# Kernel optimization log

Measured on AMD Instinct MI355X. Metric: run time of the kernel, lower is better.

## Reference

```python
import jax, jax.numpy as jnp
import numpy as np

BN_EPS = 1e-5
DIST_MIN = 1e-8
K = 3


def setup_inputs() -> dict:
    key = jax.random.key(0)
    ks = jax.random.split(key, 6)
    B, Nl, Nh, Ch, Cl, out_ch = 4, 8192, 2048, 256, 128, 256
    in_ch = Ch + Cl
    xyz_low = jax.random.normal(ks[0], (B, Nl, 3), jnp.float32)
    xyz_high = jax.random.normal(ks[1], (B, Nh, 3), jnp.float32)
    feat_low = jax.random.normal(ks[2], (B, Cl, Nl), jnp.float32)
    feat_high = jax.random.normal(ks[3], (B, Ch, Nh), jnp.float32)
    # 1x1 Conv1d params (kernel size 1 -> plain channel-mixing matrix)
    W = jax.random.normal(ks[4], (out_ch, in_ch), jnp.float32) * (1.0 / np.sqrt(in_ch))
    b = jax.random.normal(ks[5], (out_ch,), jnp.float32) * 0.01
    gamma = jnp.ones((out_ch,), jnp.float32)
    beta = jnp.zeros((out_ch,), jnp.float32)
    return {"xyz_low": xyz_low, "xyz_high": xyz_high, "feat_low": feat_low,
            "feat_high": feat_high, "W": W, "b": b, "gamma": gamma, "beta": beta}


def reference(xyz_low, xyz_high, feat_low, feat_high, W, b, gamma, beta):
    # --- pairwise euclidean distances (B, Nl, Nh), like torch.cdist ---
    d2 = (jnp.sum(xyz_low ** 2, -1)[:, :, None]
          + jnp.sum(xyz_high ** 2, -1)[:, None, :]
          - 2.0 * jnp.einsum('bld,bhd->blh', xyz_low, xyz_high))
    d = jnp.sqrt(jnp.maximum(d2, 0.0))
    # --- 3-NN (smallest distances) ---
    _, idx = jax.lax.top_k(-d, K)                      # (B, Nl, K)
    dist = jnp.maximum(jnp.take_along_axis(d, idx, axis=-1), DIST_MIN)
    w = 1.0 / dist
    w = w / jnp.sum(w, axis=-1, keepdims=True)         # (B, Nl, K)
    # --- gather neighbor features and inverse-distance interpolate ---
    f_high_T = jnp.transpose(feat_high, (0, 2, 1))      # (B, Nh, Ch)
    neigh = jax.vmap(lambda f, i: f[i])(f_high_T, idx)  # (B, Nl, K, Ch)
    f_interp = jnp.einsum('blk,blkc->bcl', w, neigh)    # (B, Ch, Nl)
    f_cat = jnp.concatenate([f_interp, feat_low], axis=1)  # (B, Ch+Cl, Nl)
    # --- 1x1 Conv1d + BatchNorm1d (training-mode batch stats) + ReLU ---
    y = jnp.einsum('oc,bcn->bon', W, f_cat) + b[None, :, None]
    mean = jnp.mean(y, axis=(0, 2), keepdims=True)
    var = jnp.var(y, axis=(0, 2), keepdims=True)        # biased, as in torch BN
    yn = (y - mean) * jax.lax.rsqrt(var + BN_EPS)
    return jax.nn.relu(gamma[None, :, None] * yn + beta[None, :, None])
```

## Files before the change

kernel.cpp:

```cpp
#include <hip/hip_runtime.h>

constexpr int B_   = 4;
constexpr int NL   = 8192;
constexpr int NH   = 2048;
constexpr int CH   = 256;
constexpr int CL   = 128;
constexpr int CIN  = 384;
constexpr int COUT = 256;

typedef _Float16 f16;
typedef _Float16 f16x8 __attribute__((ext_vector_type(8)));
typedef float    f32x4 __attribute__((ext_vector_type(4)));

#define INS3F(d, h, B0, B1, B2, I0, I1, I2) do {                             \
    bool c0_ = (d) < (B0), c1_ = (d) < (B1), c2_ = (d) < (B2);               \
    int ni1_ = c0_ ? (I0) : (c1_ ? (h) : (I1));                              \
    int ni2_ = c1_ ? (I1) : (c2_ ? (h) : (I2));                              \
    I0 = c0_ ? (h) : (I0); I1 = ni1_; I2 = ni2_;                             \
    float nb1_ = __builtin_amdgcn_fmed3f(B0, B1, (d));                       \
    float nb2_ = __builtin_amdgcn_fmed3f(B1, B2, (d));                       \
    B0 = fminf(B0, (d)); B1 = nb1_; B2 = nb2_;                               \
} while (0)

__global__ __launch_bounds__(256) void prep_kernel(
    const float* __restrict__ feat_high, const float* __restrict__ Wm,
    f16* __restrict__ fhT, f16* __restrict__ Wh)
{
    __shared__ float tt[32][33];
    const int bid = blockIdx.x, tid = threadIdx.x;

    if (bid < 512) {
        const int tx = tid & 31, ty = tid >> 5;
        #pragma unroll
        for (int k = 0; k < 4; ++k) {
            const int u  = bid * 4 + k;
            const int ub = u >> 9, ut = u & 511;
            const int h0 = (ut & 63) * 32, c0 = (ut >> 6) * 32;
            #pragma unroll
            for (int pp = 0; pp < 4; ++pp)
                tt[ty + pp * 8][tx] =
                    feat_high[((size_t)ub * CH + c0 + ty + pp * 8) * NH + h0 + tx];
            __syncthreads();
            #pragma unroll
            for (int pp = 0; pp < 4; ++pp)
                fhT[((size_t)ub * NH + h0 + ty + pp * 8) * CH + c0 + tx] =
                    (f16)tt[tx][ty + pp * 8];
            __syncthreads();
        }
    } else {
        const int i = (bid - 512) * 256 + tid;
        Wh[i] = (f16)Wm[i];
    }
}

__global__ __launch_bounds__(512) void gemm_kernel(
    const float* __restrict__ xyz_low, const float* __restrict__ xyz_high,
    const float* __restrict__ feat_low, const f16* __restrict__ fhT,
    const f16* __restrict__ Wh, const float* __restrict__ bias,
    f16* __restrict__ yh, float* __restrict__ ps, float* __restrict__ psq)
{
    __shared__ __align__(16) char smraw[51712];
    f16*            As   = (f16*)smraw;
    float4*         pts  = (float4*)smraw;
    float*          md   = (float*)(smraw + 32768);
    unsigned short* mi   = (unsigned short*)(smraw + 39168);
    int*            idxL = (int*)(smraw + 50176);
    float*          wL   = (float*)(smraw + 50944);

    const int bid = blockIdx.x, tid = threadIdx.x;
    const int b = bid >> 7, l0 = (bid & 127) * 64;
    const int lane = tid & 63, w = tid >> 6;

    {
        const float* xh = xyz_high + (size_t)b * NH * 3;
        #pragma unroll
        for (int k = 0; k < 4; ++k) {
            const int h = k * 512 + tid;
            float x = xh[h * 3], yy = xh[h * 3 + 1], z = xh[h * 3 + 2];
            pts[h] = make_float4(x, yy, z, x * x + yy * yy + z * z);
        }
    }
    __syncthreads();
    {
        const float* xl = xyz_low + ((size_t)b * NL + l0 + lane) * 3;
        const float lx = xl[0], ly = xl[1], lz = xl[2];
        const float sl = lx * lx + ly * ly + lz * lz;

        float a0 = 1e30f, a1 = 1e30f, a2 = 1e30f;
        float c0 = 1e30f, c1 = 1e30f, c2 = 1e30f;
        int ia0 = 0, ia1 = 0, ia2 = 0, ic0 = 0, ic1 = 0, ic2 = 0;
        const int hA = w * 256, hB = hA + 128;
        #pragma unroll 4
        for (int i = 0; i < 128; ++i) {
            float4 pA = pts[hA + i];
            float4 pB = pts[hB + i];
            float dA = fmaf(-2.0f, fmaf(lx, pA.x, fmaf(ly, pA.y, lz * pA.z)),
                            sl + pA.w);
            float dB = fmaf(-2.0f, fmaf(lx, pB.x, fmaf(ly, pB.y, lz * pB.z)),
                            sl + pB.w);
            INS3F(dA, hA + i, a0, a1, a2, ia0, ia1, ia2);
            INS3F(dB, hB + i, c0, c1, c2, ic0, ic1, ic2);
        }
        INS3F(c0, ic0, a0, a1, a2, ia0, ia1, ia2);
        INS3F(c1, ic1, a0, a1, a2, ia0, ia1, ia2);
        INS3F(c2, ic2, a0, a1, a2, ia0, ia1, ia2);
        const int cb = lane * 25 + w * 3;
        md[cb] = a0;     mi[cb] = (unsigned short)ia0;
        md[cb + 1] = a1; mi[cb + 1] = (unsigned short)ia1;
        md[cb + 2] = a2; mi[cb + 2] = (unsigned short)ia2;
    }
    __syncthreads();

    if (tid < 64) {
        float e0 = 1e30f, e1 = 1e30f, e2 = 1e30f;
        int j0 = 0, j1 = 0, j2 = 0;
        #pragma unroll
        for (int q = 0; q < 24; ++q) {
            float d = md[tid * 25 + q];
            int  ii = mi[tid * 25 + q];
            INS3F(d, ii, e0, e1, e2, j0, j1, j2);
        }
        float d0 = sqrtf(fmaxf(e0, 0.0f));
        float d1 = sqrtf(fmaxf(e1, 0.0f));
        float d2f = sqrtf(fmaxf(e2, 0.0f));
        float iw0 = 1.0f / fmaxf(d0, 1e-8f);
        float iw1 = 1.0f / fmaxf(d1, 1e-8f);
        float iw2 = 1.0f / fmaxf(d2f, 1e-8f);
        float sum = iw0 + iw1 + iw2;
        idxL[tid] = j0; idxL[64 + tid] = j1; idxL[128 + tid] = j2;
        wL[tid] = iw0 / sum; wL[64 + tid] = iw1 / sum; wL[128 + tid] = iw2 / sum;
    }
    __syncthreads();

    {
        const int p = tid >> 3, q = tid & 7;
        const int j0 = idxL[p], j1 = idxL[64 + p], j2 = idxL[128 + p];
        const float u0 = wL[p], u1 = wL[64 + p], u2 = wL[128 + p];
        const f16* r0 = fhT + ((size_t)b * NH + j0) * CH + q * 32;
        const f16* r1 = fhT + ((size_t)b * NH + j1) * CH + q * 32;
        const f16* r2 = fhT + ((size_t)b * NH + j2) * CH + q * 32;
        #pragma unroll
        for (int j = 0; j < 4; ++j) {
            f16x8 v0 = *(const f16x8*)(r0 + j * 8);
            f16x8 v1 = *(const f16x8*)(r1 + j * 8);
            f16x8 v2 = *(const f16x8*)(r2 + j * 8);
            f16x8 o;
            #pragma unroll
            for (int e = 0; e < 8; ++e)
                o[e] = (f16)(u0 * (float)v0[e] + u1 * (float)v1[e]
                             + u2 * (float)v2[e]);
            *(f16x8*)&As[p * 392 + q * 32 + j * 8] = o;
        }
        const int l = tid & 63, cq = tid >> 6;
        const float* flb = feat_low + ((size_t)b * CL + cq * 16) * NL + l0 + l;
        f16 tmp[16];
        #pragma unroll
        for (int i = 0; i < 16; ++i)
            tmp[i] = (f16)flb[(size_t)i * NL];
        *(f16x8*)&As[l * 392 + 256 + cq * 16]     = *(const f16x8*)&tmp[0];
        *(f16x8*)&As[l * 392 + 256 + cq * 16 + 8] = *(const f16x8*)&tmp[8];
    }
    __syncthreads();

    f32x4 acc[2][4] = {};
    const int kb = (lane >> 4) * 8;
    const int r  = lane & 15;
    #pragma unroll
    for (int kt = 0; kt < 12; ++kt) {
        const int k0 = kt * 32;
        f16x8 a[2], bb[4];
        #pragma unroll
        for (int mi2 = 0; mi2 < 2; ++mi2)
            a[mi2] = *(const f16x8*)&Wh[(size_t)(w * 32 + mi2 * 16 + r) * CIN
                                        + k0 + kb];
        #pragma unroll
        for (int ni = 0; ni < 4; ++ni)
            bb[ni] = *(const f16x8*)&As[(ni * 16 + r) * 392 + k0 + kb];
        #pragma unroll
        for (int mi2 = 0; mi2 < 2; ++mi2)
            #pragma unroll
            for (int ni = 0; ni < 4; ++ni)
                acc[mi2][ni] = __builtin_amdgcn_mfma_f32_16x16x32_f16(
                    a[mi2], bb[ni], acc[mi2][ni], 0, 0, 0);
    }

    const int r4 = (lane >> 4) * 4, cl = lane & 15;
    #pragma unroll
    for (int mi2 = 0; mi2 < 2; ++mi2) {
        #pragma unroll
        for (int j = 0; j < 4; ++j) {
            const int o = w * 32 + mi2 * 16 + r4 + j;
            const float bi = bias[o];
            float s = 0.0f, sq = 0.0f;
            #pragma unroll
            for (int ni = 0; ni < 4; ++ni) {
                acc[mi2][ni][j] += bi;
                float v = acc[mi2][ni][j];
                s += v; sq += v * v;
            }
            #pragma unroll
            for (int m = 1; m < 16; m <<= 1) {
                s  += __shfl_xor(s, m);
                sq += __shfl_xor(sq, m);
            }
            if (cl == 0) {
                ps [o * 512 + bid] = s;
                psq[o * 512 + bid] = sq;
            }
        }
    }
    __syncthreads();

    f16* Ys = (f16*)smraw;
    #pragma unroll
    for (int mi2 = 0; mi2 < 2; ++mi2)
        #pragma unroll
        for (int j = 0; j < 4; ++j) {
            const int o = w * 32 + mi2 * 16 + r4 + j;
            #pragma unroll
            for (int ni = 0; ni < 4; ++ni)
                Ys[o * 72 + cl + ni * 16] = (f16)acc[mi2][ni][j];
        }
    __syncthreads();
    {
        const int o = tid >> 1, half = tid & 1;
        f16* dst = yh + ((size_t)b * COUT + o) * NL + l0 + half * 32;
        #pragma unroll
        for (int j = 0; j < 4; ++j)
            *(f16x8*)(dst + j * 8) = *(const f16x8*)&Ys[o * 72 + half * 32 + j * 8];
    }
}

__global__ __launch_bounds__(256) void stats_apply_kernel(
    const float* __restrict__ ps, const float* __restrict__ psq,
    const f16* __restrict__ yh,
    const float* __restrict__ gamma, const float* __restrict__ beta,
    float* __restrict__ y)
{
    const int o = blockIdx.x, b = blockIdx.y, tid = threadIdx.x;
    const int w = tid >> 6, lane = tid & 63;

    float s = ps[o * 512 + tid] + ps[o * 512 + 256 + tid];
    float q = psq[o * 512 + tid] + psq[o * 512 + 256 + tid];
    #pragma unroll
    for (int m = 32; m > 0; m >>= 1) {
        s += __shfl_down(s, m);
        q += __shfl_down(q, m);
    }
    __shared__ float red[8];
    if (lane == 0) { red[w] = s; red[4 + w] = q; }
    __syncthreads();
    s = red[0] + red[1] + red[2] + red[3];
    q = red[4] + red[5] + red[6] + red[7];
    const float n  = (float)(B_ * NL);
    const float mu = s / n;
    const float rs = rsqrtf(q / n - mu * mu + 1e-5f);
    const float g  = gamma[o], be = beta[o];

    const f16* src = yh + ((size_t)b * COUT + o) * NL;
    float*     dst = y  + ((size_t)b * COUT + o) * NL;
    #pragma unroll
    for (int it = 0; it < 4; ++it) {
        const int base = it * 2048 + tid * 8;
        f16x8 v = *(const f16x8*)(src + base);
        float4 o1, o2;
        o1.x = fmaxf(fmaf(g, ((float)v[0] - mu) * rs, be), 0.0f);
        o1.y = fmaxf(fmaf(g, ((float)v[1] - mu) * rs, be), 0.0f);
        o1.z = fmaxf(fmaf(g, ((float)v[2] - mu) * rs, be), 0.0f);
        o1.w = fmaxf(fmaf(g, ((float)v[3] - mu) * rs, be), 0.0f);
        o2.x = fmaxf(fmaf(g, ((float)v[4] - mu) * rs, be), 0.0f);
        o2.y = fmaxf(fmaf(g, ((float)v[5] - mu) * rs, be), 0.0f);
        o2.z = fmaxf(fmaf(g, ((float)v[6] - mu) * rs, be), 0.0f);
        o2.w = fmaxf(fmaf(g, ((float)v[7] - mu) * rs, be), 0.0f);
        *(float4*)(dst + base)     = o1;
        *(float4*)(dst + base + 4) = o2;
    }
}

extern "C" void kernel_launch(void* const* d_in, const int* in_sizes, int n_in,
                              void* d_out, int out_size, void* d_ws, size_t ws_size,
                              hipStream_t stream)
{
    const float* xyz_low   = (const float*)d_in[0];
    const float* xyz_high  = (const float*)d_in[1];
    const float* feat_low  = (const float*)d_in[2];
    const float* feat_high = (const float*)d_in[3];
    const float* Wm        = (const float*)d_in[4];
    const float* bias      = (const float*)d_in[5];
    const float* gamma     = (const float*)d_in[6];
    const float* beta      = (const float*)d_in[7];
    float* y = (float*)d_out;

    float* ps   = (float*)d_ws;
    float* psq  = ps + (size_t)COUT * 512;
    f16*   Wh   = (f16*)(psq + (size_t)COUT * 512);
    f16*   fhT  = Wh + (size_t)COUT * CIN;
    f16*   yh   = fhT + (size_t)B_ * NH * CH;

    prep_kernel<<<896, 256, 0, stream>>>(feat_high, Wm, fhT, Wh);
    gemm_kernel<<<512, 512, 0, stream>>>(
        xyz_low, xyz_high, feat_low, fhT, Wh, bias, yh, ps, psq);
    stats_apply_kernel<<<dim3(COUT, B_), 256, 0, stream>>>(
        ps, psq, yh, gamma, beta, y);
}
```

Before: 75.82 us.

## Double gemm_kernel block size to 1024 threads and split work across 16 waves

Launches the fused kNN+GEMM kernel with 1024 threads (16 waves) instead of 512, so each wave scans 128 high-res points with a single top-3 chain and handles 16 output channels instead of 32. The merge step now reduces 48 partial candidates per point, and the gather, feat_low load and output store are re-partitioned across the larger block. The aim is more parallelism and latency hiding per block. The cost is a longer serial merge by 64 threads, slightly more LDS, and tighter register limits from the 1024-thread launch bound.

```diff
diff --git a/kernel.cpp b/kernel.cpp
--- a/kernel.cpp
+++ b/kernel.cpp
@@ -53,19 +53,19 @@
     }
 }
 
-__global__ __launch_bounds__(512) void gemm_kernel(
+__global__ __launch_bounds__(1024, 8) void gemm_kernel(
     const float* __restrict__ xyz_low, const float* __restrict__ xyz_high,
     const float* __restrict__ feat_low, const f16* __restrict__ fhT,
     const f16* __restrict__ Wh, const float* __restrict__ bias,
     f16* __restrict__ yh, float* __restrict__ ps, float* __restrict__ psq)
 {
-    __shared__ __align__(16) char smraw[51712];
+    __shared__ __align__(16) char smraw[53120];
     f16*            As   = (f16*)smraw;
     float4*         pts  = (float4*)smraw;
     float*          md   = (float*)(smraw + 32768);
-    unsigned short* mi   = (unsigned short*)(smraw + 39168);
-    int*            idxL = (int*)(smraw + 50176);
-    float*          wL   = (float*)(smraw + 50944);
+    unsigned short* mi   = (unsigned short*)(smraw + 45312);
+    int*            idxL = (int*)(smraw + 51584);
+    float*          wL   = (float*)(smraw + 52352);
 
     const int bid = blockIdx.x, tid = threadIdx.x;
     const int b = bid >> 7, l0 = (bid & 127) * 64;
@@ -74,8 +74,8 @@
     {
         const float* xh = xyz_high + (size_t)b * NH * 3;
         #pragma unroll
-        for (int k = 0; k < 4; ++k) {
-            const int h = k * 512 + tid;
+        for (int k = 0; k < 2; ++k) {
+            const int h = k * 1024 + tid;
             float x = xh[h * 3], yy = xh[h * 3 + 1], z = xh[h * 3 + 2];
             pts[h] = make_float4(x, yy, z, x * x + yy * yy + z * z);
         }
@@ -87,24 +87,16 @@
         const float sl = lx * lx + ly * ly + lz * lz;
 
         float a0 = 1e30f, a1 = 1e30f, a2 = 1e30f;
-        float c0 = 1e30f, c1 = 1e30f, c2 = 1e30f;
-        int ia0 = 0, ia1 = 0, ia2 = 0, ic0 = 0, ic1 = 0, ic2 = 0;
-        const int hA = w * 256, hB = hA + 128;
-        #pragma unroll 4
+        int ia0 = 0, ia1 = 0, ia2 = 0;
+        const int h0 = w * 128;
+        #pragma unroll 8
         for (int i = 0; i < 128; ++i) {
-            float4 pA = pts[hA + i];
-            float4 pB = pts[hB + i];
+            float4 pA = pts[h0 + i];
             float dA = fmaf(-2.0f, fmaf(lx, pA.x, fmaf(ly, pA.y, lz * pA.z)),
                             sl + pA.w);
-            float dB = fmaf(-2.0f, fmaf(lx, pB.x, fmaf(ly, pB.y, lz * pB.z)),
-                            sl + pB.w);
-            INS3F(dA, hA + i, a0, a1, a2, ia0, ia1, ia2);
-            INS3F(dB, hB + i, c0, c1, c2, ic0, ic1, ic2);
-        }
-        INS3F(c0, ic0, a0, a1, a2, ia0, ia1, ia2);
-        INS3F(c1, ic1, a0, a1, a2, ia0, ia1, ia2);
-        INS3F(c2, ic2, a0, a1, a2, ia0, ia1, ia2);
-        const int cb = lane * 25 + w * 3;
+            INS3F(dA, h0 + i, a0, a1, a2, ia0, ia1, ia2);
+        }
+        const int cb = lane * 49 + w * 3;
         md[cb] = a0;     mi[cb] = (unsigned short)ia0;
         md[cb + 1] = a1; mi[cb + 1] = (unsigned short)ia1;
         md[cb + 2] = a2; mi[cb + 2] = (unsigned short)ia2;
@@ -115,9 +107,9 @@
         float e0 = 1e30f, e1 = 1e30f, e2 = 1e30f;
         int j0 = 0, j1 = 0, j2 = 0;
         #pragma unroll
-        for (int q = 0; q < 24; ++q) {
-            float d = md[tid * 25 + q];
-            int  ii = mi[tid * 25 + q];
+        for (int q = 0; q < 48; ++q) {
+            float d = md[tid * 49 + q];
+            int  ii = mi[tid * 49 + q];
             INS3F(d, ii, e0, e1, e2, j0, j1, j2);
         }
         float d0 = sqrtf(fmaxf(e0, 0.0f));
@@ -133,14 +125,14 @@
     __syncthreads();
 
     {
-        const int p = tid >> 3, q = tid & 7;
+        const int p = tid >> 4, q = tid & 15;
         const int j0 = idxL[p], j1 = idxL[64 + p], j2 = idxL[128 + p];
         const float u0 = wL[p], u1 = wL[64 + p], u2 = wL[128 + p];
-        const f16* r0 = fhT + ((size_t)b * NH + j0) * CH + q * 32;
-        const f16* r1 = fhT + ((size_t)b * NH + j1) * CH + q * 32;
-        const f16* r2 = fhT + ((size_t)b * NH + j2) * CH + q * 32;
-        #pragma unroll
-        for (int j = 0; j < 4; ++j) {
+        const f16* r0 = fhT + ((size_t)b * NH + j0) * CH + q * 16;
+        const f16* r1 = fhT + ((size_t)b * NH + j1) * CH + q * 16;
+        const f16* r2 = fhT + ((size_t)b * NH + j2) * CH + q * 16;
+        #pragma unroll
+        for (int j = 0; j < 2; ++j) {
             f16x8 v0 = *(const f16x8*)(r0 + j * 8);
             f16x8 v1 = *(const f16x8*)(r1 + j * 8);
             f16x8 v2 = *(const f16x8*)(r2 + j * 8);
@@ -149,85 +141,73 @@
             for (int e = 0; e < 8; ++e)
                 o[e] = (f16)(u0 * (float)v0[e] + u1 * (float)v1[e]
                              + u2 * (float)v2[e]);
-            *(f16x8*)&As[p * 392 + q * 32 + j * 8] = o;
+            *(f16x8*)&As[p * 392 + q * 16 + j * 8] = o;
         }
         const int l = tid & 63, cq = tid >> 6;
-        const float* flb = feat_low + ((size_t)b * CL + cq * 16) * NL + l0 + l;
-        f16 tmp[16];
-        #pragma unroll
-        for (int i = 0; i < 16; ++i)
+        const float* flb = feat_low + ((size_t)b * CL + cq * 8) * NL + l0 + l;
+        f16 tmp[8];
+        #pragma unroll
+        for (int i = 0; i < 8; ++i)
             tmp[i] = (f16)flb[(size_t)i * NL];
-        *(f16x8*)&As[l * 392 + 256 + cq * 16]     = *(const f16x8*)&tmp[0];
-        *(f16x8*)&As[l * 392 + 256 + cq * 16 + 8] = *(const f16x8*)&tmp[8];
-    }
-    __syncthreads();
-
-    f32x4 acc[2][4] = {};
+        *(f16x8*)&As[l * 392 + 256 + cq * 8] = *(const f16x8*)&tmp[0];
+    }
+    __syncthreads();
+
+    f32x4 acc[4] = {};
     const int kb = (lane >> 4) * 8;
     const int r  = lane & 15;
     #pragma unroll
     for (int kt = 0; kt < 12; ++kt) {
         const int k0 = kt * 32;
-        f16x8 a[2], bb[4];
-        #pragma unroll
-        for (int mi2 = 0; mi2 < 2; ++mi2)
-            a[mi2] = *(const f16x8*)&Wh[(size_t)(w * 32 + mi2 * 16 + r) * CIN
-                                        + k0 + kb];
+        f16x8 a = *(const f16x8*)&Wh[(size_t)(w * 16 + r) * CIN + k0 + kb];
+        f16x8 bb[4];
         #pragma unroll
         for (int ni = 0; ni < 4; ++ni)
             bb[ni] = *(const f16x8*)&As[(ni * 16 + r) * 392 + k0 + kb];
         #pragma unroll
-        for (int mi2 = 0; mi2 < 2; ++mi2)
-            #pragma unroll
-            for (int ni = 0; ni < 4; ++ni)
-                acc[mi2][ni] = __builtin_amdgcn_mfma_f32_16x16x32_f16(
-                    a[mi2], bb[ni], acc[mi2][ni], 0, 0, 0);
+        for (int ni = 0; ni < 4; ++ni)
+            acc[ni] = __builtin_amdgcn_mfma_f32_16x16x32_f16(
+                a, bb[ni], acc[ni], 0, 0, 0);
     }
 
     const int r4 = (lane >> 4) * 4, cl = lane & 15;
     #pragma unroll
-    for (int mi2 = 0; mi2 < 2; ++mi2) {
-        #pragma unroll
-        for (int j = 0; j < 4; ++j) {
-            const int o = w * 32 + mi2 * 16 + r4 + j;
-            const float bi = bias[o];
-            float s = 0.0f, sq = 0.0f;
-            #pragma unroll
-            for (int ni = 0; ni < 4; ++ni) {
-                acc[mi2][ni][j] += bi;
-                float v = acc[mi2][ni][j];
-                s += v; sq += v * v;
-            }
-            #pragma unroll
-            for (int m = 1; m < 16; m <<= 1) {
-                s  += __shfl_xor(s, m);
-                sq += __shfl_xor(sq, m);
-            }
-            if (cl == 0) {
-                ps [o * 512 + bid] = s;
-                psq[o * 512 + bid] = sq;
-            }
+    for (int j = 0; j < 4; ++j) {
+        const int o = w * 16 + r4 + j;
+        const float bi = bias[o];
+        float s = 0.0f, sq = 0.0f;
+        #pragma unroll
+        for (int ni = 0; ni < 4; ++ni) {
+            acc[ni][j] += bi;
+            float v = acc[ni][j];
+            s += v; sq += v * v;
+        }
+        #pragma unroll
+        for (int m = 1; m < 16; m <<= 1) {
+            s  += __shfl_xor(s, m);
+            sq += __shfl_xor(sq, m);
+        }
+        if (cl == 0) {
+            ps [o * 512 + bid] = s;
+            psq[o * 512 + bid] = sq;
         }
     }
     __syncthreads();
 
     f16* Ys = (f16*)smraw;
     #pragma unroll
-    for (int mi2 = 0; mi2 < 2; ++mi2)
-        #pragma unroll
-        for (int j = 0; j < 4; ++j) {
-            const int o = w * 32 + mi2 * 16 + r4 + j;
-            #pragma unroll
-            for (int ni = 0; ni < 4; ++ni)
-                Ys[o * 72 + cl + ni * 16] = (f16)acc[mi2][ni][j];
-        }
-    __syncthreads();
-    {
-        const int o = tid >> 1, half = tid & 1;
-        f16* dst = yh + ((size_t)b * COUT + o) * NL + l0 + half * 32;
-        #pragma unroll
-        for (int j = 0; j < 4; ++j)
-            *(f16x8*)(dst + j * 8) = *(const f16x8*)&Ys[o * 72 + half * 32 + j * 8];
+    for (int j = 0; j < 4; ++j) {
+        const int o = w * 16 + r4 + j;
+        #pragma unroll
+        for (int ni = 0; ni < 4; ++ni)
+            Ys[o * 72 + cl + ni * 16] = (f16)acc[ni][j];
+    }
+    __syncthreads();
+    {
+        const int o = tid >> 2, qtr = tid & 3;
+        f16* dst = yh + ((size_t)b * COUT + o) * NL + l0 + qtr * 16;
+        *(f16x8*)(dst)     = *(const f16x8*)&Ys[o * 72 + qtr * 16];
+        *(f16x8*)(dst + 8) = *(const f16x8*)&Ys[o * 72 + qtr * 16 + 8];
     }
 }
 
@@ -298,7 +278,7 @@
     f16*   yh   = fhT + (size_t)B_ * NH * CH;
 
     prep_kernel<<<896, 256, 0, stream>>>(feat_high, Wm, fhT, Wh);
-    gemm_kernel<<<512, 512, 0, stream>>>(
+    gemm_kernel<<<512, 1024, 0, stream>>>(
         xyz_low, xyz_high, feat_low, fhT, Wh, bias, yh, ps, psq);
     stats_apply_kernel<<<dim3(COUT, B_), 256, 0, stream>>>(
         ps, psq, yh, gamma, beta, y);
```

Result: faster. 66.98 us (-11.7%).
